# Kernel optimization log

Measured on AMD Instinct MI355X. Metric: run time of the kernel, lower is better.

## Reference

```python
import jax, jax.numpy as jnp
import numpy as np

EPS = 1e-8  # torch CosineSimilarity default eps

def _mlp2(h, W1, b1, W2, b2):
    # two-layer MLP with ReLU after each linear
    h = jax.nn.relu(h @ W1 + b1)
    return jax.nn.relu(h @ W2 + b2)

def setup_inputs() -> dict:
    key = jax.random.key(0)
    ks = jax.random.split(key, 24)
    N, E, D, O, P = 65536, 131072, 256, 128, 32
    inp = {
        "x": jax.random.normal(ks[0], (N, D), dtype=jnp.float32),
        "edge_index": jax.random.randint(ks[1], (2, E), 0, N, dtype=jnp.int64),
        "edge_attr": jax.random.normal(ks[2], (E, P), dtype=jnp.float32),
    }
    sD = 1.0 / np.sqrt(D)
    for i, name in enumerate(["1", "2", "3", "4"]):
        inp[f"W{name}a"] = jax.random.normal(ks[3 + 4 * i], (D, D), dtype=jnp.float32) * sD
        inp[f"b{name}a"] = jnp.zeros((D,), dtype=jnp.float32)
        inp[f"W{name}b"] = jax.random.normal(ks[4 + 4 * i], (D, O), dtype=jnp.float32) * sD
        inp[f"b{name}b"] = jnp.zeros((O,), dtype=jnp.float32)
    Fin = 1 + 4 * O + P  # 545
    inp["Wf"] = jax.random.normal(ks[20], (Fin, O), dtype=jnp.float32) / np.sqrt(Fin)
    inp["bf"] = jnp.zeros((O,), dtype=jnp.float32)
    return inp

def reference(x, edge_index, edge_attr,
              W1a, b1a, W1b, b1b,
              W2a, b2a, W2b, b2b,
              W3a, b3a, W3b, b3b,
              W4a, b4a, W4b, b4b,
              Wf, bf):
    x_src = x[edge_index[0]]  # [E, D]
    x_dst = x[edge_index[1]]  # [E, D]
    y = jnp.concatenate([
        _mlp2(x_src, W1a, b1a, W1b, b1b),
        _mlp2(x_dst, W2a, b2a, W2b, b2b),
        _mlp2(x_src - x_dst, W3a, b3a, W3b, b3b),
        _mlp2(x_src * x_dst, W4a, b4a, W4b, b4b),
    ], axis=1)  # [E, 4*O]
    # cosine similarity over feature dim (torch dim=1 after unsqueeze(2)) -> [E, 1]
    ns = jnp.maximum(jnp.linalg.norm(x_src, axis=1, keepdims=True), EPS)
    nd = jnp.maximum(jnp.linalg.norm(x_dst, axis=1, keepdims=True), EPS)
    s = jnp.sum((x_src / ns) * (x_dst / nd), axis=1, keepdims=True)  # [E, 1]
    z = jnp.concatenate([y, s, edge_attr], axis=1)  # [E, 1+4*O+P]
    return jnp.tanh(z @ Wf + bf)  # [E, O]
```

## Files before the change

kernel.cpp:

```cpp
#include <hip/hip_runtime.h>
#include <hip/hip_bf16.h>

typedef unsigned short u16;
typedef __attribute__((ext_vector_type(8))) short short8;
typedef __attribute__((ext_vector_type(4))) float f32x4;

#define NE 131072

#define OFF_WA 0
#define OFF_WB 262144
#define OFF_WF 393216
#define OFF_WE 458752
#define OFF_WS 462848

#define ASYNC16(gp, lp) __builtin_amdgcn_global_load_lds( \
    (const __attribute__((address_space(1))) unsigned int*)(gp), \
    (__attribute__((address_space(3))) unsigned int*)(lp), 16, 0, 0)
#define LGKM0() __builtin_amdgcn_s_waitcnt(0xC07F)
#define WAIT2() asm volatile("s_waitcnt vmcnt(2)" ::: "memory")
#define VM0()   asm volatile("s_waitcnt vmcnt(0)" ::: "memory")

__device__ __forceinline__ float b2f(u16 v) {
    unsigned int u = ((unsigned int)v) << 16;
    float f;
    __builtin_memcpy(&f, &u, 4);
    return f;
}
__device__ __forceinline__ u16 f2b(float f) {
    __hip_bfloat16 h = __float2bfloat16(f);
    u16 u;
    __builtin_memcpy(&u, &h, 2);
    return u;
}
__device__ __forceinline__ short8 pack8(f32x4 a, f32x4 b) {
    short8 p;
    p[0] = (short)f2b(a.x); p[1] = (short)f2b(a.y);
    p[2] = (short)f2b(a.z); p[3] = (short)f2b(a.w);
    p[4] = (short)f2b(b.x); p[5] = (short)f2b(b.y);
    p[6] = (short)f2b(b.z); p[7] = (short)f2b(b.w);
    return p;
}

#define MFMA16(a, b, c) __builtin_amdgcn_mfma_f32_16x16x32_bf16(a, b, c, 0, 0, 0)

struct BiasP {
    const float* ba[4];
    const float* bb[4];
};

__device__ __forceinline__ void issue_chunk(const u16* __restrict__ ws, u16* Wb,
                                            int wave, int lane, int gc) {
    if (gc >= 112) return;
    const int m = gc / 28;
    const int c = gc - m * 28;
    const int r = lane >> 2;
    const int slot = (lane & 3) ^ ((lane >> 3) & 3);
    u16* lp = Wb + wave * 2048 + (gc & 1) * 1024;
    const u16* gp;
    int rstride;
    if (c < 16) {
        int kk = c >> 1, nh = c & 1;
        gp = ws + OFF_WA + m * 65536
           + (size_t)(wave * 64 + nh * 32 + r) * 256 + kk * 32 + slot * 8;
        rstride = 16 * 256;
    } else if (c < 24) {
        int kc = c - 16;
        gp = ws + OFF_WB + m * 32768
           + (size_t)(wave * 32 + r) * 256 + kc * 32 + slot * 8;
        rstride = 16 * 256;
    } else {
        int cc = c - 24;
        gp = ws + OFF_WF + m * 16384
           + (size_t)(wave * 32 + r) * 128 + cc * 32 + slot * 8;
        rstride = 16 * 128;
    }
    ASYNC16(gp, lp);
    ASYNC16(gp + rstride, lp + 512);
}

__global__ __launch_bounds__(256)
void prep_kernel(const float* __restrict__ W1a, const float* __restrict__ W2a,
                 const float* __restrict__ W3a, const float* __restrict__ W4a,
                 const float* __restrict__ W1b, const float* __restrict__ W2b,
                 const float* __restrict__ W3b, const float* __restrict__ W4b,
                 const float* __restrict__ Wf,  u16* __restrict__ ws) {
    __shared__ __align__(16) u16 T[64 * 80];

    const int y = blockIdx.y;
    const int t = threadIdx.x;
    const float* in;
    int K, N;
    if (y < 4)      { in = (y == 0) ? W1a : (y == 1) ? W2a : (y == 2) ? W3a : W4a; K = 256; N = 256; }
    else if (y < 8) { in = (y == 4) ? W1b : (y == 5) ? W2b : (y == 6) ? W3b : W4b; K = 256; N = 128; }
    else            { in = Wf; K = 545; N = 128; }

    const int ntilesN = N / 64;
    const int ktiles = (K + 63) / 64;
    const int kt = blockIdx.x / ntilesN;
    const int nt = blockIdx.x - kt * ntilesN;
    if (kt >= ktiles) return;
    const int kbase = kt * 64, nbase = nt * 64;

    {
        int tn = (t & 15) * 4;
        int tk = t >> 4;
        #pragma unroll
        for (int r = 0; r < 4; r++) {
            int k = kbase + tk + 16 * r;
            if (k < K) {
                float4 v = *(const float4*)(in + (size_t)k * N + nbase + tn);
                T[(tn + 0) * 80 + tk + 16 * r] = f2b(v.x);
                T[(tn + 1) * 80 + tk + 16 * r] = f2b(v.y);
                T[(tn + 2) * 80 + tk + 16 * r] = f2b(v.z);
                T[(tn + 3) * 80 + tk + 16 * r] = f2b(v.w);
            }
        }
    }
    __syncthreads();
    {
        int n = t >> 2;
        int kc = (t & 3) * 16;
        int n_out = nbase + n;
        const u16* src = &T[n * 80 + kc];
        if (y < 4) {
            u16* dst = ws + OFF_WA + y * 65536 + (size_t)n_out * 256 + kbase + kc;
            *(short8*)dst = *(const short8*)src;
            *(short8*)(dst + 8) = *(const short8*)(src + 8);
        } else if (y < 8) {
            u16* dst = ws + OFF_WB + (y - 4) * 32768 + (size_t)n_out * 256 + kbase + kc;
            *(short8*)dst = *(const short8*)src;
            *(short8*)(dst + 8) = *(const short8*)(src + 8);
        } else if (kbase < 512) {
            u16* dst = ws + OFF_WF + (kbase >> 7) * 16384 + (size_t)n_out * 128 + (kbase & 127) + kc;
            *(short8*)dst = *(const short8*)src;
            *(short8*)(dst + 8) = *(const short8*)(src + 8);
        } else {
            #pragma unroll
            for (int j = 0; j < 16; j++) {
                int k = kbase + kc + j;
                if (k < 545) {
                    u16 v = src[j];
                    if (k == 512)      ws[OFF_WS + n_out] = v;
                    else               ws[OFF_WE + n_out * 32 + (k - 513)] = v;
                }
            }
        }
    }
}

__global__ __launch_bounds__(256, 2)
void fused_kernel(const float* __restrict__ x, const int* __restrict__ ei,
                  const float* __restrict__ ea, const u16* __restrict__ ws,
                  BiasP bp, const float* __restrict__ bfp, float* __restrict__ out) {
    __shared__ __align__(16) u16 Xs[32][264];
    __shared__ __align__(16) u16 Xd[32][264];
    __shared__ __align__(16) u16 Hs[32][264];
    __shared__ __align__(16) u16 Gs[32][136];
    __shared__ __align__(16) u16 Wb[8192];
    __shared__ float scos[32];

    const int t = threadIdx.x;
    const int wave = t >> 6;
    const int lane = t & 63;
    const int l15 = lane & 15;
    const int g = lane >> 4;
    const int e0 = blockIdx.x * 32;
    const f32x4 zero4 = {0.f, 0.f, 0.f, 0.f};

    bool idx64 = true;
    #pragma unroll
    for (int i = 1; i < 16; i += 2) { idx64 = idx64 && (ei[i] == 0); }

    const int colA = wave * 64;
    const int colC = wave * 32;

    short8 eaA[2];
    #pragma unroll
    for (int mt = 0; mt < 2; mt++) {
        const float* er = ea + (size_t)(e0 + mt * 16 + l15) * 32 + g * 8;
        f32x4 a = *(const f32x4*)(er);
        f32x4 b = *(const f32x4*)(er + 4);
        eaA[mt] = pack8(a, b);
    }
    short8 eaB[2];
    float epi_b[2], epi_w[2];
    #pragma unroll
    for (int nt = 0; nt < 2; nt++) {
        int col = colC + nt * 16 + l15;
        eaB[nt] = *(const short8*)(ws + OFF_WE + col * 32 + g * 8);
        epi_b[nt] = bfp[col];
        epi_w[nt] = b2f(ws[OFF_WS + col]);
    }
    float biasA[4][4], biasB[4][2];
    #pragma unroll
    for (int m = 0; m < 4; m++) {
        #pragma unroll
        for (int nt = 0; nt < 4; nt++) biasA[m][nt] = bp.ba[m][colA + nt * 16 + l15];
        #pragma unroll
        for (int nt = 0; nt < 2; nt++) biasB[m][nt] = bp.bb[m][colC + nt * 16 + l15];
    }

    issue_chunk(ws, Wb, wave, lane, 0);
    issue_chunk(ws, Wb, wave, lane, 1);

    {
        int edge = t >> 3;
        int c = t & 7;
        int pos = e0 + edge;
        int is = idx64 ? ei[2 * pos] : ei[pos];
        int id = idx64 ? ei[2 * (NE + pos)] : ei[NE + pos];
        const float* rs = x + (size_t)is * 256 + c * 32;
        const float* rd = x + (size_t)id * 256 + c * 32;
        float dot = 0.f, ss = 0.f, dd = 0.f;
        #pragma unroll
        for (int i = 0; i < 4; i++) {
            f32x4 s0 = *(const f32x4*)(rs + i * 8);
            f32x4 s1 = *(const f32x4*)(rs + i * 8 + 4);
            f32x4 d0 = *(const f32x4*)(rd + i * 8);
            f32x4 d1 = *(const f32x4*)(rd + i * 8 + 4);
            dot += s0.x * d0.x + s0.y * d0.y + s0.z * d0.z + s0.w * d0.w
                 + s1.x * d1.x + s1.y * d1.y + s1.z * d1.z + s1.w * d1.w;
            ss  += s0.x * s0.x + s0.y * s0.y + s0.z * s0.z + s0.w * s0.w
                 + s1.x * s1.x + s1.y * s1.y + s1.z * s1.z + s1.w * s1.w;
            dd  += d0.x * d0.x + d0.y * d0.y + d0.z * d0.z + d0.w * d0.w
                 + d1.x * d1.x + d1.y * d1.y + d1.z * d1.z + d1.w * d1.w;
            *(short8*)(&Xs[edge][c * 32 + i * 8]) = pack8(s0, s1);
            *(short8*)(&Xd[edge][c * 32 + i * 8]) = pack8(d0, d1);
        }
        dot += __shfl_xor(dot, 1); ss += __shfl_xor(ss, 1); dd += __shfl_xor(dd, 1);
        dot += __shfl_xor(dot, 2); ss += __shfl_xor(ss, 2); dd += __shfl_xor(dd, 2);
        dot += __shfl_xor(dot, 4); ss += __shfl_xor(ss, 4); dd += __shfl_xor(dd, 4);
        if (c == 0) {
            float ns = fmaxf(sqrtf(ss), 1e-8f);
            float nd = fmaxf(sqrtf(dd), 1e-8f);
            scos[edge] = dot / (ns * nd);
        }
    }
    __syncthreads();

    const u16* xsb0 = &Xs[l15][g * 8];      const u16* xsb1 = &Xs[16 + l15][g * 8];
    const u16* xdb0 = &Xd[l15][g * 8];      const u16* xdb1 = &Xd[16 + l15][g * 8];
    const u16* hrb0 = &Hs[l15][g * 8];      const u16* hrb1 = &Hs[16 + l15][g * 8];
    const u16* grb0 = &Gs[l15][g * 8];      const u16* grb1 = &Gs[16 + l15][g * 8];
    const u16* wbase = Wb + wave * 2048 + l15 * 32 + ((g ^ ((l15 >> 1) & 3)) * 8);

    f32x4 Facc[2][2];
    #pragma unroll
    for (int a = 0; a < 2; a++) {
        #pragma unroll
        for (int b = 0; b < 2; b++) Facc[a][b] = zero4;
    }

    #pragma unroll
    for (int m = 0; m < 4; m++) {
        f32x4 accA[2][4];
        #pragma unroll
        for (int a = 0; a < 2; a++) {
            #pragma unroll
            for (int b = 0; b < 4; b++) accA[a][b] = zero4;
        }
        #pragma unroll
        for (int kk = 0; kk < 8; kk++) {
            const int gc = m * 28 + kk * 2;
            short8 s0, s1, d0, d1;
            if (m != 1) { s0 = *(const short8*)(xsb0 + kk * 32); s1 = *(const short8*)(xsb1 + kk * 32); }
            if (m != 0) { d0 = *(const short8*)(xdb0 + kk * 32); d1 = *(const short8*)(xdb1 + kk * 32); }
            WAIT2();
            const u16* wq0 = wbase + (gc & 1) * 1024;
            short8 wf0 = *(const short8*)(wq0);
            short8 wf1 = *(const short8*)(wq0 + 512);
            LGKM0();
            issue_chunk(ws, Wb, wave, lane, gc + 2);
            short8 af0, af1;
            if (m == 0)      { af0 = s0; af1 = s1; }
            else if (m == 1) { af0 = d0; af1 = d1; }
            else {
                #pragma unroll
                for (int mt = 0; mt < 2; mt++) {
                    short8 s = mt ? s1 : s0, d = mt ? d1 : d0, rr;
                    #pragma unroll
                    for (int j = 0; j < 8; j++) {
                        float fs = b2f((u16)s[j]);
                        float fd = b2f((u16)d[j]);
                        rr[j] = (short)f2b((m == 2) ? (fs - fd) : (fs * fd));
                    }
                    if (mt) af1 = rr; else af0 = rr;
                }
            }
            accA[0][0] = MFMA16(af0, wf0, accA[0][0]);
            accA[1][0] = MFMA16(af1, wf0, accA[1][0]);
            accA[0][1] = MFMA16(af0, wf1, accA[0][1]);
            accA[1][1] = MFMA16(af1, wf1, accA[1][1]);
            WAIT2();
            const u16* wq1 = wbase + ((gc + 1) & 1) * 1024;
            short8 wf2 = *(const short8*)(wq1);
            short8 wf3 = *(const short8*)(wq1 + 512);
            LGKM0();
            issue_chunk(ws, Wb, wave, lane, gc + 3);
            accA[0][2] = MFMA16(af0, wf2, accA[0][2]);
            accA[1][2] = MFMA16(af1, wf2, accA[1][2]);
            accA[0][3] = MFMA16(af0, wf3, accA[0][3]);
            accA[1][3] = MFMA16(af1, wf3, accA[1][3]);
        }
        #pragma unroll
        for (int nt = 0; nt < 4; nt++) {
            int col = colA + nt * 16 + l15;
            #pragma unroll
            for (int mt = 0; mt < 2; mt++) {
                #pragma unroll
                for (int rg = 0; rg < 4; rg++) {
                    int row = mt * 16 + g * 4 + rg;
                    Hs[row][col] = f2b(fmaxf(accA[mt][nt][rg] + biasA[m][nt], 0.f));
                }
            }
        }
        __syncthreads();

        f32x4 accB[2][2];
        #pragma unroll
        for (int a = 0; a < 2; a++) {
            #pragma unroll
            for (int b = 0; b < 2; b++) accB[a][b] = zero4;
        }
        #pragma unroll
        for (int kc = 0; kc < 8; kc++) {
            const int gc = m * 28 + 16 + kc;
            short8 hf0 = *(const short8*)(hrb0 + kc * 32);
            short8 hf1 = *(const short8*)(hrb1 + kc * 32);
            WAIT2();
            const u16* wq = wbase + (gc & 1) * 1024;
            short8 wf0 = *(const short8*)(wq);
            short8 wf1 = *(const short8*)(wq + 512);
            LGKM0();
            issue_chunk(ws, Wb, wave, lane, gc + 2);
            accB[0][0] = MFMA16(hf0, wf0, accB[0][0]);
            accB[1][0] = MFMA16(hf1, wf0, accB[1][0]);
            accB[0][1] = MFMA16(hf0, wf1, accB[0][1]);
            accB[1][1] = MFMA16(hf1, wf1, accB[1][1]);
        }
        #pragma unroll
        for (int nt = 0; nt < 2; nt++) {
            int col = colC + nt * 16 + l15;
            #pragma unroll
            for (int mt = 0; mt < 2; mt++) {
                #pragma unroll
                for (int rg = 0; rg < 4; rg++) {
                    int row = mt * 16 + g * 4 + rg;
                    Gs[row][col] = f2b(fmaxf(accB[mt][nt][rg] + biasB[m][nt], 0.f));
                }
            }
        }
        __syncthreads();

        #pragma unroll
        for (int cc = 0; cc < 4; cc++) {
            const int gc = m * 28 + 24 + cc;
            short8 gf0 = *(const short8*)(grb0 + cc * 32);
            short8 gf1 = *(const short8*)(grb1 + cc * 32);
            if (m == 3 && cc == 3) { VM0(); } else { WAIT2(); }
            const u16* wq = wbase + (gc & 1) * 1024;
            short8 wf0 = *(const short8*)(wq);
            short8 wf1 = *(const short8*)(wq + 512);
            LGKM0();
            issue_chunk(ws, Wb, wave, lane, gc + 2);
            Facc[0][0] = MFMA16(gf0, wf0, Facc[0][0]);
            Facc[1][0] = MFMA16(gf1, wf0, Facc[1][0]);
            Facc[0][1] = MFMA16(gf0, wf1, Facc[0][1]);
            Facc[1][1] = MFMA16(gf1, wf1, Facc[1][1]);
        }
    }

    #pragma unroll
    for (int mt = 0; mt < 2; mt++) {
        #pragma unroll
        for (int nt = 0; nt < 2; nt++) {
            Facc[mt][nt] = MFMA16(eaA[mt], eaB[nt], Facc[mt][nt]);
        }
    }

    float* os = (float*)&Xs[0][0];
    #pragma unroll
    for (int nt = 0; nt < 2; nt++) {
        int col = colC + nt * 16 + l15;
        #pragma unroll
        for (int mt = 0; mt < 2; mt++) {
            #pragma unroll
            for (int rg = 0; rg < 4; rg++) {
                int row = mt * 16 + g * 4 + rg;
                float v = Facc[mt][nt][rg] + scos[row] * epi_w[nt] + epi_b[nt];
                v = fminf(fmaxf(v, -15.f), 15.f);
                float e2 = __expf(2.f * v);
                os[row * 132 + col] = (e2 - 1.f) / (e2 + 1.f);
            }
        }
    }
    __syncthreads();
    {
        int row = t >> 3, c = t & 7;
        float* op = out + (size_t)(e0 + row) * 128 + c * 16;
        const float* sp = os + row * 132 + c * 16;
        #pragma unroll
        for (int i = 0; i < 4; i++) {
            f32x4 v = *(const f32x4*)(sp + i * 4);
            *(f32x4*)(op + i * 4) = v;
        }
    }
}

extern "C" void kernel_launch(void* const* d_in, const int* in_sizes, int n_in,
                              void* d_out, int out_size, void* d_ws, size_t ws_size,
                              hipStream_t stream) {
    u16* ws = (u16*)d_ws;
    prep_kernel<<<dim3(18, 9), 256, 0, stream>>>(
        (const float*)d_in[3],  (const float*)d_in[7],  (const float*)d_in[11], (const float*)d_in[15],
        (const float*)d_in[5],  (const float*)d_in[9],  (const float*)d_in[13], (const float*)d_in[17],
        (const float*)d_in[19], ws);

    BiasP bp;
    bp.ba[0] = (const float*)d_in[4];  bp.ba[1] = (const float*)d_in[8];
    bp.ba[2] = (const float*)d_in[12]; bp.ba[3] = (const float*)d_in[16];
    bp.bb[0] = (const float*)d_in[6];  bp.bb[1] = (const float*)d_in[10];
    bp.bb[2] = (const float*)d_in[14]; bp.bb[3] = (const float*)d_in[18];

    fused_kernel<<<NE / 32, 256, 0, stream>>>(
        (const float*)d_in[0], (const int*)d_in[1], (const float*)d_in[2], ws,
        bp, (const float*)d_in[20], (float*)d_out);
}
```

Baseline: 428.3 us.

## Load MLP weights directly into registers and drop the LDS weight staging buffer

The async global-to-LDS weight chunk pipeline (Wb buffer with vmcnt waits) is removed. Each wave now loads its MFMA B-operand weight fragments straight from global memory into registers, double-buffered two k-steps ahead. The Gs buffer is merged into Hs, and bias and edge-attribute loads are moved to the point of use. Together these cut LDS use and register pressure so launch bounds can rise from 2 to 3 blocks per CU. The trade-off is uncoalesced 16-byte global loads per lane whose latency is hidden only by the shallow register prefetch and the higher occupancy.

```diff
diff --git a/kernel.cpp b/kernel.cpp
--- a/kernel.cpp
+++ b/kernel.cpp
@@ -12,13 +12,6 @@
 #define OFF_WF 393216
 #define OFF_WE 458752
 #define OFF_WS 462848
-
-#define ASYNC16(gp, lp) __builtin_amdgcn_global_load_lds( \
-    (const __attribute__((address_space(1))) unsigned int*)(gp), \
-    (__attribute__((address_space(3))) unsigned int*)(lp), 16, 0, 0)
-#define LGKM0() __builtin_amdgcn_s_waitcnt(0xC07F)
-#define WAIT2() asm volatile("s_waitcnt vmcnt(2)" ::: "memory")
-#define VM0()   asm volatile("s_waitcnt vmcnt(0)" ::: "memory")
 
 __device__ __forceinline__ float b2f(u16 v) {
     unsigned int u = ((unsigned int)v) << 16;
@@ -47,36 +40,6 @@
     const float* ba[4];
     const float* bb[4];
 };
-
-__device__ __forceinline__ void issue_chunk(const u16* __restrict__ ws, u16* Wb,
-                                            int wave, int lane, int gc) {
-    if (gc >= 112) return;
-    const int m = gc / 28;
-    const int c = gc - m * 28;
-    const int r = lane >> 2;
-    const int slot = (lane & 3) ^ ((lane >> 3) & 3);
-    u16* lp = Wb + wave * 2048 + (gc & 1) * 1024;
-    const u16* gp;
-    int rstride;
-    if (c < 16) {
-        int kk = c >> 1, nh = c & 1;
-        gp = ws + OFF_WA + m * 65536
-           + (size_t)(wave * 64 + nh * 32 + r) * 256 + kk * 32 + slot * 8;
-        rstride = 16 * 256;
-    } else if (c < 24) {
-        int kc = c - 16;
-        gp = ws + OFF_WB + m * 32768
-           + (size_t)(wave * 32 + r) * 256 + kc * 32 + slot * 8;
-        rstride = 16 * 256;
-    } else {
-        int cc = c - 24;
-        gp = ws + OFF_WF + m * 16384
-           + (size_t)(wave * 32 + r) * 128 + cc * 32 + slot * 8;
-        rstride = 16 * 128;
-    }
-    ASYNC16(gp, lp);
-    ASYNC16(gp + rstride, lp + 512);
-}
 
 __global__ __launch_bounds__(256)
 void prep_kernel(const float* __restrict__ W1a, const float* __restrict__ W2a,
@@ -148,15 +111,13 @@
     }
 }
 
-__global__ __launch_bounds__(256, 2)
+__global__ __launch_bounds__(256, 3)
 void fused_kernel(const float* __restrict__ x, const int* __restrict__ ei,
                   const float* __restrict__ ea, const u16* __restrict__ ws,
                   BiasP bp, const float* __restrict__ bfp, float* __restrict__ out) {
     __shared__ __align__(16) u16 Xs[32][264];
     __shared__ __align__(16) u16 Xd[32][264];
     __shared__ __align__(16) u16 Hs[32][264];
-    __shared__ __align__(16) u16 Gs[32][136];
-    __shared__ __align__(16) u16 Wb[8192];
     __shared__ float scos[32];
 
     const int t = threadIdx.x;
@@ -166,42 +127,22 @@
     const int g = lane >> 4;
     const int e0 = blockIdx.x * 32;
     const f32x4 zero4 = {0.f, 0.f, 0.f, 0.f};
-
-    bool idx64 = true;
-    #pragma unroll
-    for (int i = 1; i < 16; i += 2) { idx64 = idx64 && (ei[i] == 0); }
-
     const int colA = wave * 64;
     const int colC = wave * 32;
 
-    short8 eaA[2];
-    #pragma unroll
-    for (int mt = 0; mt < 2; mt++) {
-        const float* er = ea + (size_t)(e0 + mt * 16 + l15) * 32 + g * 8;
-        f32x4 a = *(const f32x4*)(er);
-        f32x4 b = *(const f32x4*)(er + 4);
-        eaA[mt] = pack8(a, b);
-    }
-    short8 eaB[2];
-    float epi_b[2], epi_w[2];
-    #pragma unroll
-    for (int nt = 0; nt < 2; nt++) {
-        int col = colC + nt * 16 + l15;
-        eaB[nt] = *(const short8*)(ws + OFF_WE + col * 32 + g * 8);
-        epi_b[nt] = bfp[col];
-        epi_w[nt] = b2f(ws[OFF_WS + col]);
-    }
-    float biasA[4][4], biasB[4][2];
-    #pragma unroll
-    for (int m = 0; m < 4; m++) {
-        #pragma unroll
-        for (int nt = 0; nt < 4; nt++) biasA[m][nt] = bp.ba[m][colA + nt * 16 + l15];
-        #pragma unroll
-        for (int nt = 0; nt < 2; nt++) biasB[m][nt] = bp.bb[m][colC + nt * 16 + l15];
-    }
-
-    issue_chunk(ws, Wb, wave, lane, 0);
-    issue_chunk(ws, Wb, wave, lane, 1);
+    bool idx64 = true;
+    #pragma unroll
+    for (int i = 1; i < 16; i += 2) { idx64 = idx64 && (ei[i] == 0); }
+
+    const u16* pA = ws + OFF_WA + (size_t)(colA + l15) * 256 + g * 8;
+    const u16* pB = ws + OFF_WB + (size_t)(colC + l15) * 256 + g * 8;
+    const u16* pC = ws + OFF_WF + (size_t)(colC + l15) * 128 + g * 8;
+
+    short8 wfA[2][4];
+    #pragma unroll
+    for (int nt = 0; nt < 4; nt++) wfA[0][nt] = *(const short8*)(pA + nt * 4096);
+    #pragma unroll
+    for (int nt = 0; nt < 4; nt++) wfA[1][nt] = *(const short8*)(pA + nt * 4096 + 32);
 
     {
         int edge = t >> 3;
@@ -240,9 +181,7 @@
 
     const u16* xsb0 = &Xs[l15][g * 8];      const u16* xsb1 = &Xs[16 + l15][g * 8];
     const u16* xdb0 = &Xd[l15][g * 8];      const u16* xdb1 = &Xd[16 + l15][g * 8];
-    const u16* hrb0 = &Hs[l15][g * 8];      const u16* hrb1 = &Hs[16 + l15][g * 8];
-    const u16* grb0 = &Gs[l15][g * 8];      const u16* grb1 = &Gs[16 + l15][g * 8];
-    const u16* wbase = Wb + wave * 2048 + l15 * 32 + ((g ^ ((l15 >> 1) & 3)) * 8);
+    const u16* hgb0 = &Hs[l15][g * 8];      const u16* hgb1 = &Hs[16 + l15][g * 8];
 
     f32x4 Facc[2][2];
     #pragma unroll
@@ -253,6 +192,16 @@
 
     #pragma unroll
     for (int m = 0; m < 4; m++) {
+        const u16* pAm = pA + m * 65536;
+        const u16* pBm = pB + m * 32768;
+        const u16* pCm = pC + m * 16384;
+        float biasA_m[4];
+        #pragma unroll
+        for (int nt = 0; nt < 4; nt++) biasA_m[nt] = bp.ba[m][colA + nt * 16 + l15];
+        float biasB_m[2];
+        #pragma unroll
+        for (int nt = 0; nt < 2; nt++) biasB_m[nt] = bp.bb[m][colC + nt * 16 + l15];
+
         f32x4 accA[2][4];
         #pragma unroll
         for (int a = 0; a < 2; a++) {
@@ -261,16 +210,16 @@
         }
         #pragma unroll
         for (int kk = 0; kk < 8; kk++) {
-            const int gc = m * 28 + kk * 2;
+            short8 w0 = wfA[kk & 1][0], w1 = wfA[kk & 1][1];
+            short8 w2 = wfA[kk & 1][2], w3 = wfA[kk & 1][3];
+            if (kk < 6) {
+                #pragma unroll
+                for (int nt = 0; nt < 4; nt++)
+                    wfA[kk & 1][nt] = *(const short8*)(pAm + nt * 4096 + (kk + 2) * 32);
+            }
             short8 s0, s1, d0, d1;
             if (m != 1) { s0 = *(const short8*)(xsb0 + kk * 32); s1 = *(const short8*)(xsb1 + kk * 32); }
             if (m != 0) { d0 = *(const short8*)(xdb0 + kk * 32); d1 = *(const short8*)(xdb1 + kk * 32); }
-            WAIT2();
-            const u16* wq0 = wbase + (gc & 1) * 1024;
-            short8 wf0 = *(const short8*)(wq0);
-            short8 wf1 = *(const short8*)(wq0 + 512);
-            LGKM0();
-            issue_chunk(ws, Wb, wave, lane, gc + 2);
             short8 af0, af1;
             if (m == 0)      { af0 = s0; af1 = s1; }
             else if (m == 1) { af0 = d0; af1 = d1; }
@@ -287,21 +236,20 @@
                     if (mt) af1 = rr; else af0 = rr;
                 }
             }
-            accA[0][0] = MFMA16(af0, wf0, accA[0][0]);
-            accA[1][0] = MFMA16(af1, wf0, accA[1][0]);
-            accA[0][1] = MFMA16(af0, wf1, accA[0][1]);
-            accA[1][1] = MFMA16(af1, wf1, accA[1][1]);
-            WAIT2();
-            const u16* wq1 = wbase + ((gc + 1) & 1) * 1024;
-            short8 wf2 = *(const short8*)(wq1);
-            short8 wf3 = *(const short8*)(wq1 + 512);
-            LGKM0();
-            issue_chunk(ws, Wb, wave, lane, gc + 3);
-            accA[0][2] = MFMA16(af0, wf2, accA[0][2]);
-            accA[1][2] = MFMA16(af1, wf2, accA[1][2]);
-            accA[0][3] = MFMA16(af0, wf3, accA[0][3]);
-            accA[1][3] = MFMA16(af1, wf3, accA[1][3]);
-        }
+            accA[0][0] = MFMA16(af0, w0, accA[0][0]);
+            accA[1][0] = MFMA16(af1, w0, accA[1][0]);
+            accA[0][1] = MFMA16(af0, w1, accA[0][1]);
+            accA[1][1] = MFMA16(af1, w1, accA[1][1]);
+            accA[0][2] = MFMA16(af0, w2, accA[0][2]);
+            accA[1][2] = MFMA16(af1, w2, accA[1][2]);
+            accA[0][3] = MFMA16(af0, w3, accA[0][3]);
+            accA[1][3] = MFMA16(af1, w3, accA[1][3]);
+        }
+        short8 wfB[2][2];
+        wfB[0][0] = *(const short8*)(pBm);
+        wfB[0][1] = *(const short8*)(pBm + 4096);
+        wfB[1][0] = *(const short8*)(pBm + 32);
+        wfB[1][1] = *(const short8*)(pBm + 4096 + 32);
         #pragma unroll
         for (int nt = 0; nt < 4; nt++) {
             int col = colA + nt * 16 + l15;
@@ -310,7 +258,7 @@
                 #pragma unroll
                 for (int rg = 0; rg < 4; rg++) {
                     int row = mt * 16 + g * 4 + rg;
-                    Hs[row][col] = f2b(fmaxf(accA[mt][nt][rg] + biasA[m][nt], 0.f));
+                    Hs[row][col] = f2b(fmaxf(accA[mt][nt][rg] + biasA_m[nt], 0.f));
                 }
             }
         }
@@ -324,20 +272,24 @@
         }
         #pragma unroll
         for (int kc = 0; kc < 8; kc++) {
-            const int gc = m * 28 + 16 + kc;
-            short8 hf0 = *(const short8*)(hrb0 + kc * 32);
-            short8 hf1 = *(const short8*)(hrb1 + kc * 32);
-            WAIT2();
-            const u16* wq = wbase + (gc & 1) * 1024;
-            short8 wf0 = *(const short8*)(wq);
-            short8 wf1 = *(const short8*)(wq + 512);
-            LGKM0();
-            issue_chunk(ws, Wb, wave, lane, gc + 2);
-            accB[0][0] = MFMA16(hf0, wf0, accB[0][0]);
-            accB[1][0] = MFMA16(hf1, wf0, accB[1][0]);
-            accB[0][1] = MFMA16(hf0, wf1, accB[0][1]);
-            accB[1][1] = MFMA16(hf1, wf1, accB[1][1]);
-        }
+            short8 w0 = wfB[kc & 1][0], w1 = wfB[kc & 1][1];
+            if (kc < 6) {
+                wfB[kc & 1][0] = *(const short8*)(pBm + (kc + 2) * 32);
+                wfB[kc & 1][1] = *(const short8*)(pBm + 4096 + (kc + 2) * 32);
+            }
+            short8 hf0 = *(const short8*)(hgb0 + kc * 32);
+            short8 hf1 = *(const short8*)(hgb1 + kc * 32);
+            accB[0][0] = MFMA16(hf0, w0, accB[0][0]);
+            accB[1][0] = MFMA16(hf1, w0, accB[1][0]);
+            accB[0][1] = MFMA16(hf0, w1, accB[0][1]);
+            accB[1][1] = MFMA16(hf1, w1, accB[1][1]);
+        }
+        short8 wfC[2][2];
+        wfC[0][0] = *(const short8*)(pCm);
+        wfC[0][1] = *(const short8*)(pCm + 2048);
+        wfC[1][0] = *(const short8*)(pCm + 32);
+        wfC[1][1] = *(const short8*)(pCm + 2048 + 32);
+        __syncthreads();
         #pragma unroll
         for (int nt = 0; nt < 2; nt++) {
             int col = colC + nt * 16 + l15;
@@ -346,7 +298,7 @@
                 #pragma unroll
                 for (int rg = 0; rg < 4; rg++) {
                     int row = mt * 16 + g * 4 + rg;
-                    Gs[row][col] = f2b(fmaxf(accB[mt][nt][rg] + biasB[m][nt], 0.f));
+                    Hs[row][col] = f2b(fmaxf(accB[mt][nt][rg] + biasB_m[nt], 0.f));
                 }
             }
         }
@@ -354,29 +306,51 @@
 
         #pragma unroll
         for (int cc = 0; cc < 4; cc++) {
-            const int gc = m * 28 + 24 + cc;
-            short8 gf0 = *(const short8*)(grb0 + cc * 32);
-            short8 gf1 = *(const short8*)(grb1 + cc * 32);
-            if (m == 3 && cc == 3) { VM0(); } else { WAIT2(); }
-            const u16* wq = wbase + (gc & 1) * 1024;
-            short8 wf0 = *(const short8*)(wq);
-            short8 wf1 = *(const short8*)(wq + 512);
-            LGKM0();
-            issue_chunk(ws, Wb, wave, lane, gc + 2);
-            Facc[0][0] = MFMA16(gf0, wf0, Facc[0][0]);
-            Facc[1][0] = MFMA16(gf1, wf0, Facc[1][0]);
-            Facc[0][1] = MFMA16(gf0, wf1, Facc[0][1]);
-            Facc[1][1] = MFMA16(gf1, wf1, Facc[1][1]);
-        }
-    }
-
-    #pragma unroll
-    for (int mt = 0; mt < 2; mt++) {
-        #pragma unroll
-        for (int nt = 0; nt < 2; nt++) {
-            Facc[mt][nt] = MFMA16(eaA[mt], eaB[nt], Facc[mt][nt]);
-        }
-    }
+            short8 w0 = wfC[cc & 1][0], w1 = wfC[cc & 1][1];
+            if (cc < 2) {
+                wfC[cc & 1][0] = *(const short8*)(pCm + (cc + 2) * 32);
+                wfC[cc & 1][1] = *(const short8*)(pCm + 2048 + (cc + 2) * 32);
+            }
+            short8 gf0 = *(const short8*)(hgb0 + cc * 32);
+            short8 gf1 = *(const short8*)(hgb1 + cc * 32);
+            Facc[0][0] = MFMA16(gf0, w0, Facc[0][0]);
+            Facc[1][0] = MFMA16(gf1, w0, Facc[1][0]);
+            Facc[0][1] = MFMA16(gf0, w1, Facc[0][1]);
+            Facc[1][1] = MFMA16(gf1, w1, Facc[1][1]);
+        }
+        if (m < 3) {
+            #pragma unroll
+            for (int nt = 0; nt < 4; nt++)
+                wfA[0][nt] = *(const short8*)(pAm + 65536 + nt * 4096);
+            #pragma unroll
+            for (int nt = 0; nt < 4; nt++)
+                wfA[1][nt] = *(const short8*)(pAm + 65536 + nt * 4096 + 32);
+            __syncthreads();
+        }
+    }
+
+    short8 eaA0, eaA1, eaB0, eaB1;
+    float epi_b[2], epi_w[2];
+    {
+        const float* er0 = ea + (size_t)(e0 + l15) * 32 + g * 8;
+        const float* er1 = ea + (size_t)(e0 + 16 + l15) * 32 + g * 8;
+        f32x4 a0 = *(const f32x4*)(er0);
+        f32x4 b0 = *(const f32x4*)(er0 + 4);
+        f32x4 a1 = *(const f32x4*)(er1);
+        f32x4 b1 = *(const f32x4*)(er1 + 4);
+        eaA0 = pack8(a0, b0);
+        eaA1 = pack8(a1, b1);
+        eaB0 = *(const short8*)(ws + OFF_WE + (colC + l15) * 32 + g * 8);
+        eaB1 = *(const short8*)(ws + OFF_WE + (colC + 16 + l15) * 32 + g * 8);
+        epi_b[0] = bfp[colC + l15];
+        epi_b[1] = bfp[colC + 16 + l15];
+        epi_w[0] = b2f(ws[OFF_WS + colC + l15]);
+        epi_w[1] = b2f(ws[OFF_WS + colC + 16 + l15]);
+    }
+    Facc[0][0] = MFMA16(eaA0, eaB0, Facc[0][0]);
+    Facc[1][0] = MFMA16(eaA1, eaB0, Facc[1][0]);
+    Facc[0][1] = MFMA16(eaA0, eaB1, Facc[0][1]);
+    Facc[1][1] = MFMA16(eaA1, eaB1, Facc[1][1]);
 
     float* os = (float*)&Xs[0][0];
     #pragma unroll
```

Result: slower. 592.8 us (+38.4%).

## Triple-buffer weight chunk prefetch and alias G buffer onto H in LDS

Applied to the files above, without the earlier changes.

Deepens the per-wave weight staging ring from two to three LDS chunks, prefetching three chunks ahead with matching vmcnt waits so global-to-LDS loads have more time in flight. The separate Gs buffer is removed and the layer output reuses Hs, which adds barriers around the write. Barriers become raw s_barrier after lgkmcnt(0) rather than __syncthreads, skipping a full vmcnt drain so async weight loads stay outstanding. LDS use stays roughly flat, but the extra barriers add synchronisation and the new wait counts must stay correct for the tail chunks.

```diff
diff --git a/kernel.cpp b/kernel.cpp
--- a/kernel.cpp
+++ b/kernel.cpp
@@ -17,8 +17,10 @@
     (const __attribute__((address_space(1))) unsigned int*)(gp), \
     (__attribute__((address_space(3))) unsigned int*)(lp), 16, 0, 0)
 #define LGKM0() __builtin_amdgcn_s_waitcnt(0xC07F)
+#define WAIT4() asm volatile("s_waitcnt vmcnt(4)" ::: "memory")
 #define WAIT2() asm volatile("s_waitcnt vmcnt(2)" ::: "memory")
-#define VM0()   asm volatile("s_waitcnt vmcnt(0)" ::: "memory")
+#define WAIT0() asm volatile("s_waitcnt vmcnt(0)" ::: "memory")
+#define BAR() asm volatile("s_waitcnt lgkmcnt(0)\n\ts_barrier" ::: "memory")
 
 __device__ __forceinline__ float b2f(u16 v) {
     unsigned int u = ((unsigned int)v) << 16;
@@ -55,7 +57,7 @@
     const int c = gc - m * 28;
     const int r = lane >> 2;
     const int slot = (lane & 3) ^ ((lane >> 3) & 3);
-    u16* lp = Wb + wave * 2048 + (gc & 1) * 1024;
+    u16* lp = Wb + wave * 3072 + (gc % 3) * 1024;
     const u16* gp;
     int rstride;
     if (c < 16) {
@@ -155,8 +157,7 @@
     __shared__ __align__(16) u16 Xs[32][264];
     __shared__ __align__(16) u16 Xd[32][264];
     __shared__ __align__(16) u16 Hs[32][264];
-    __shared__ __align__(16) u16 Gs[32][136];
-    __shared__ __align__(16) u16 Wb[8192];
+    __shared__ __align__(16) u16 Wb[12288];
     __shared__ float scos[32];
 
     const int t = threadIdx.x;
@@ -166,13 +167,12 @@
     const int g = lane >> 4;
     const int e0 = blockIdx.x * 32;
     const f32x4 zero4 = {0.f, 0.f, 0.f, 0.f};
-
-    bool idx64 = true;
-    #pragma unroll
-    for (int i = 1; i < 16; i += 2) { idx64 = idx64 && (ei[i] == 0); }
-
     const int colA = wave * 64;
     const int colC = wave * 32;
+
+    bool idx64 = true;
+    #pragma unroll
+    for (int i = 1; i < 16; i += 2) { idx64 = idx64 && (ei[i] == 0); }
 
     short8 eaA[2];
     #pragma unroll
@@ -202,6 +202,7 @@
 
     issue_chunk(ws, Wb, wave, lane, 0);
     issue_chunk(ws, Wb, wave, lane, 1);
+    issue_chunk(ws, Wb, wave, lane, 2);
 
     {
         int edge = t >> 3;
@@ -236,13 +237,12 @@
             scos[edge] = dot / (ns * nd);
         }
     }
-    __syncthreads();
+    BAR();
 
     const u16* xsb0 = &Xs[l15][g * 8];      const u16* xsb1 = &Xs[16 + l15][g * 8];
     const u16* xdb0 = &Xd[l15][g * 8];      const u16* xdb1 = &Xd[16 + l15][g * 8];
-    const u16* hrb0 = &Hs[l15][g * 8];      const u16* hrb1 = &Hs[16 + l15][g * 8];
-    const u16* grb0 = &Gs[l15][g * 8];      const u16* grb1 = &Gs[16 + l15][g * 8];
-    const u16* wbase = Wb + wave * 2048 + l15 * 32 + ((g ^ ((l15 >> 1) & 3)) * 8);
+    const u16* hgb0 = &Hs[l15][g * 8];      const u16* hgb1 = &Hs[16 + l15][g * 8];
+    const u16* wbase = Wb + wave * 3072 + l15 * 32 + ((g ^ ((l15 >> 1) & 3)) * 8);
 
     f32x4 Facc[2][2];
     #pragma unroll
@@ -265,12 +265,12 @@
             short8 s0, s1, d0, d1;
             if (m != 1) { s0 = *(const short8*)(xsb0 + kk * 32); s1 = *(const short8*)(xsb1 + kk * 32); }
             if (m != 0) { d0 = *(const short8*)(xdb0 + kk * 32); d1 = *(const short8*)(xdb1 + kk * 32); }
-            WAIT2();
-            const u16* wq0 = wbase + (gc & 1) * 1024;
+            WAIT4();
+            const u16* wq0 = wbase + (gc % 3) * 1024;
             short8 wf0 = *(const short8*)(wq0);
             short8 wf1 = *(const short8*)(wq0 + 512);
             LGKM0();
-            issue_chunk(ws, Wb, wave, lane, gc + 2);
+            issue_chunk(ws, Wb, wave, lane, gc + 3);
             short8 af0, af1;
             if (m == 0)      { af0 = s0; af1 = s1; }
             else if (m == 1) { af0 = d0; af1 = d1; }
@@ -291,12 +291,12 @@
             accA[1][0] = MFMA16(af1, wf0, accA[1][0]);
             accA[0][1] = MFMA16(af0, wf1, accA[0][1]);
             accA[1][1] = MFMA16(af1, wf1, accA[1][1]);
-            WAIT2();
-            const u16* wq1 = wbase + ((gc + 1) & 1) * 1024;
+            WAIT4();
+            const u16* wq1 = wbase + ((gc + 1) % 3) * 1024;
             short8 wf2 = *(const short8*)(wq1);
             short8 wf3 = *(const short8*)(wq1 + 512);
             LGKM0();
-            issue_chunk(ws, Wb, wave, lane, gc + 3);
+            issue_chunk(ws, Wb, wave, lane, gc + 4);
             accA[0][2] = MFMA16(af0, wf2, accA[0][2]);
             accA[1][2] = MFMA16(af1, wf2, accA[1][2]);
             accA[0][3] = MFMA16(af0, wf3, accA[0][3]);
@@ -314,7 +314,7 @@
                 }
             }
         }
-        __syncthreads();
+        BAR();
 
         f32x4 accB[2][2];
         #pragma unroll
@@ -325,19 +325,20 @@
         #pragma unroll
         for (int kc = 0; kc < 8; kc++) {
             const int gc = m * 28 + 16 + kc;
-            short8 hf0 = *(const short8*)(hrb0 + kc * 32);
-            short8 hf1 = *(const short8*)(hrb1 + kc * 32);
-            WAIT2();
-            const u16* wq = wbase + (gc & 1) * 1024;
+            short8 hf0 = *(const short8*)(hgb0 + kc * 32);
+            short8 hf1 = *(const short8*)(hgb1 + kc * 32);
+            WAIT4();
+            const u16* wq = wbase + (gc % 3) * 1024;
             short8 wf0 = *(const short8*)(wq);
             short8 wf1 = *(const short8*)(wq + 512);
             LGKM0();
-            issue_chunk(ws, Wb, wave, lane, gc + 2);
+            issue_chunk(ws, Wb, wave, lane, gc + 3);
             accB[0][0] = MFMA16(hf0, wf0, accB[0][0]);
             accB[1][0] = MFMA16(hf1, wf0, accB[1][0]);
             accB[0][1] = MFMA16(hf0, wf1, accB[0][1]);
             accB[1][1] = MFMA16(hf1, wf1, accB[1][1]);
         }
+        BAR();
         #pragma unroll
         for (int nt = 0; nt < 2; nt++) {
             int col = colC + nt * 16 + l15;
@@ -346,28 +347,31 @@
                 #pragma unroll
                 for (int rg = 0; rg < 4; rg++) {
                     int row = mt * 16 + g * 4 + rg;
-                    Gs[row][col] = f2b(fmaxf(accB[mt][nt][rg] + biasB[m][nt], 0.f));
+                    Hs[row][col] = f2b(fmaxf(accB[mt][nt][rg] + biasB[m][nt], 0.f));
                 }
             }
         }
-        __syncthreads();
+        BAR();
 
         #pragma unroll
         for (int cc = 0; cc < 4; cc++) {
             const int gc = m * 28 + 24 + cc;
-            short8 gf0 = *(const short8*)(grb0 + cc * 32);
-            short8 gf1 = *(const short8*)(grb1 + cc * 32);
-            if (m == 3 && cc == 3) { VM0(); } else { WAIT2(); }
-            const u16* wq = wbase + (gc & 1) * 1024;
+            short8 gf0 = *(const short8*)(hgb0 + cc * 32);
+            short8 gf1 = *(const short8*)(hgb1 + cc * 32);
+            if (m == 3 && cc == 2)      { WAIT2(); }
+            else if (m == 3 && cc == 3) { WAIT0(); }
+            else                        { WAIT4(); }
+            const u16* wq = wbase + (gc % 3) * 1024;
             short8 wf0 = *(const short8*)(wq);
             short8 wf1 = *(const short8*)(wq + 512);
             LGKM0();
-            issue_chunk(ws, Wb, wave, lane, gc + 2);
+            issue_chunk(ws, Wb, wave, lane, gc + 3);
             Facc[0][0] = MFMA16(gf0, wf0, Facc[0][0]);
             Facc[1][0] = MFMA16(gf1, wf0, Facc[1][0]);
             Facc[0][1] = MFMA16(gf0, wf1, Facc[0][1]);
             Facc[1][1] = MFMA16(gf1, wf1, Facc[1][1]);
         }
+        if (m < 3) BAR();
     }
 
     #pragma unroll
@@ -394,7 +398,7 @@
             }
         }
     }
-    __syncthreads();
+    BAR();
     {
         int row = t >> 3, c = t & 7;
         float* op = out + (size_t)(e0 + row) * 128 + c * 16;
```

Result: no change. 421.5 us (-1.6%).
